# Optimization experiments

Measured on AMD Instinct MI355X. Metric: run time of the kernel, lower is better.

Reference implementation:

```python
import jax, jax.numpy as jnp
import numpy as np

N_NODES = 100000
N_EDGES = 400000
DIM = 3
HID = 32


def _glorot(key, shape):
    fan_in, fan_out = shape[0], shape[1]
    lim = np.sqrt(6.0 / (fan_in + fan_out))
    return jax.random.uniform(key, shape, jnp.float32, -lim, lim)


def setup_inputs() -> dict:
    key = jax.random.key(0)
    ks = jax.random.split(key, 12)
    x = jax.random.normal(ks[0], (N_NODES, DIM), jnp.float32)
    edge_index = jax.random.randint(ks[1], (2, N_EDGES), 0, N_NODES, jnp.int64)
    edge_attr = jax.random.normal(ks[2], (N_EDGES, DIM), jnp.float32)
    params = {
        # conv1: NNConv(3 -> 32), edge nn = Linear(3, 3*32)
        'Wn1': _glorot(ks[3], (DIM, DIM * HID)), 'bn1': jnp.zeros((DIM * HID,), jnp.float32),
        'root1': _glorot(ks[4], (DIM, HID)), 'b1': jnp.zeros((HID,), jnp.float32),
        # conv2: NNConv(32 -> 32), edge nn = Linear(3, 32*32)
        'Wn2': _glorot(ks[5], (DIM, HID * HID)), 'bn2': jnp.zeros((HID * HID,), jnp.float32),
        'root2': _glorot(ks[6], (HID, HID)), 'b2': jnp.zeros((HID,), jnp.float32),
        # fc layers
        'Wf1': _glorot(ks[7], (HID, HID)), 'bf1': jnp.zeros((HID,), jnp.float32),
        'Wf2': _glorot(ks[8], (HID, 1)), 'bf2': jnp.zeros((1,), jnp.float32),
    }
    return {'x': x, 'edge_index': edge_index, 'edge_attr': edge_attr, **params}


def _nnconv(x, src, dst, edge_attr, Wn, bn, root, b, in_c, out_c):
    # per-edge weight matrix from edge MLP: [E, in_c, out_c]
    We = (edge_attr @ Wn + bn).reshape(-1, in_c, out_c)
    # gather source features, per-edge matmul, scatter-add to destinations
    msg = jnp.einsum('ei,eio->eo', x[src], We)  # [E, out_c]
    agg = jax.ops.segment_sum(msg, dst, num_segments=x.shape[0])  # [N, out_c]
    return agg + x @ root + b


def reference(x, edge_index, edge_attr, Wn1, bn1, root1, b1, Wn2, bn2, root2, b2, Wf1, bf1, Wf2, bf2):
    src, dst = edge_index[0], edge_index[1]
    h = jax.nn.relu(_nnconv(x, src, dst, edge_attr, Wn1, bn1, root1, b1, DIM, HID))
    h = jax.nn.relu(_nnconv(h, src, dst, edge_attr, Wn2, bn2, root2, b2, HID, HID))
    h = jax.nn.relu(h @ Wf1 + bf1)
    return h @ Wf2 + bf2  # [N, 1]
```

## Files before the change

### kernel.cpp

```cpp
#include <hip/hip_runtime.h>

#define N_NODES 100000
#define N_EDGES 400000
#define SCAN_BLOCKS ((N_NODES + 255) / 256)

__global__ __launch_bounds__(256) void hist_kernel(const int* __restrict__ ei,
                                                   int* __restrict__ deg) {
    int e = blockIdx.x * 256 + threadIdx.x;
    if (e < N_EDGES) atomicAdd(&deg[ei[N_EDGES + e]], 1);
}

__global__ __launch_bounds__(256) void scanA_kernel(const int* __restrict__ deg,
                                                    int* __restrict__ rowptr,
                                                    int* __restrict__ psum) {
    __shared__ int sm[256];
    int i = blockIdx.x * 256 + threadIdx.x;
    int v = (i < N_NODES) ? deg[i] : 0;
    sm[threadIdx.x] = v;
    __syncthreads();
    #pragma unroll
    for (int off = 1; off < 256; off <<= 1) {
        int t = (threadIdx.x >= off) ? sm[threadIdx.x - off] : 0;
        __syncthreads();
        sm[threadIdx.x] += t;
        __syncthreads();
    }
    if (i < N_NODES) rowptr[i] = sm[threadIdx.x] - v;
    if (threadIdx.x == 255) psum[blockIdx.x] = sm[255];
}

__global__ __launch_bounds__(512) void scanB_kernel(int* __restrict__ psum) {
    __shared__ int sm[512];
    int i = threadIdx.x;
    int v = (i < SCAN_BLOCKS) ? psum[i] : 0;
    sm[i] = v;
    __syncthreads();
    #pragma unroll
    for (int off = 1; off < 512; off <<= 1) {
        int t = (i >= off) ? sm[i - off] : 0;
        __syncthreads();
        sm[i] += t;
        __syncthreads();
    }
    if (i < SCAN_BLOCKS) psum[i] = sm[i];
}

__global__ __launch_bounds__(256) void scanC_kernel(const int* __restrict__ psum,
                                                    int* __restrict__ rowptr,
                                                    int* __restrict__ cursor) {
    int i = blockIdx.x * 256 + threadIdx.x;
    if (i < N_NODES) {
        int base = (blockIdx.x > 0) ? psum[blockIdx.x - 1] : 0;
        int r = rowptr[i] + base;
        rowptr[i] = r;
        cursor[i] = r;
    }
    if (i == 0) rowptr[N_NODES] = N_EDGES;
}

__global__ __launch_bounds__(256) void scatter_kernel(const int* __restrict__ ei,
                                                      const float* __restrict__ ea,
                                                      int* __restrict__ cursor,
                                                      float4* __restrict__ edata) {
    int e = blockIdx.x * 256 + threadIdx.x;
    if (e >= N_EDGES) return;
    int s = ei[e], d = ei[N_EDGES + e];
    int pos = atomicAdd(&cursor[d], 1);
    edata[pos] = make_float4(ea[e*3], ea[e*3+1], ea[e*3+2], __int_as_float(s));
}

__global__ __launch_bounds__(256) void conv1_kernel(const int* __restrict__ rowptr,
                                                    const float4* __restrict__ edata,
                                                    const float* __restrict__ x,
                                                    const float* __restrict__ Wn1,
                                                    const float* __restrict__ bn1,
                                                    const float* __restrict__ root1,
                                                    const float* __restrict__ b1,
                                                    float* __restrict__ h1) {
    int gid = blockIdx.x * 256 + threadIdx.x;
    int n = gid >> 5, o = gid & 31;
    if (n >= N_NODES) return;
    float W[3][3], bb[3];
    #pragma unroll
    for (int d2 = 0; d2 < 3; ++d2)
        #pragma unroll
        for (int d = 0; d < 3; ++d) W[d2][d] = Wn1[d2*96 + d*32 + o];
    #pragma unroll
    for (int d = 0; d < 3; ++d) bb[d] = bn1[d*32 + o];

    float acc = 0.f;
    int j0 = rowptr[n], j1 = rowptr[n + 1];
    for (int j = j0; j < j1; ++j) {
        float4 ed = edata[j];
        int s = __float_as_int(ed.w);
        float x0 = x[s*3], x1 = x[s*3+1], x2 = x[s*3+2];
        float wd0 = fmaf(ed.x, W[0][0], fmaf(ed.y, W[1][0], fmaf(ed.z, W[2][0], bb[0])));
        float wd1 = fmaf(ed.x, W[0][1], fmaf(ed.y, W[1][1], fmaf(ed.z, W[2][1], bb[1])));
        float wd2 = fmaf(ed.x, W[0][2], fmaf(ed.y, W[1][2], fmaf(ed.z, W[2][2], bb[2])));
        acc += fmaf(x0, wd0, fmaf(x1, wd1, x2 * wd2));
    }
    float v = acc + b1[o];
    v = fmaf(x[n*3],   root1[o],      v);
    v = fmaf(x[n*3+1], root1[32 + o], v);
    v = fmaf(x[n*3+2], root1[64 + o], v);
    h1[(size_t)n*32 + o] = fmaxf(v, 0.f);
}

__global__ __launch_bounds__(256) void prep2_kernel(const float* __restrict__ h1,
                                                    const float* __restrict__ Wn2,
                                                    const float* __restrict__ bn2,
                                                    float4* __restrict__ G2) {
    int o = threadIdx.x & 31;
    float w0[32], w1[32], w2[32], w3[32];
    #pragma unroll
    for (int i = 0; i < 32; ++i) {
        w0[i] = Wn2[         i*32 + o];
        w1[i] = Wn2[1024 +   i*32 + o];
        w2[i] = Wn2[2048 +   i*32 + o];
        w3[i] = bn2[         i*32 + o];
    }
    int g = (blockIdx.x * 256 + threadIdx.x) >> 5;
    int gstep = (gridDim.x * 256) >> 5;
    for (int n = g; n < N_NODES; n += gstep) {
        const float* __restrict__ hr = h1 + (size_t)n * 32;
        float g0 = 0.f, g1 = 0.f, g2 = 0.f, g3 = 0.f;
        #pragma unroll
        for (int i = 0; i < 32; ++i) {
            float hi = hr[i];
            g0 = fmaf(hi, w0[i], g0);
            g1 = fmaf(hi, w1[i], g1);
            g2 = fmaf(hi, w2[i], g2);
            g3 = fmaf(hi, w3[i], g3);
        }
        G2[(size_t)n*32 + o] = make_float4(g0, g1, g2, g3);
    }
}

__global__ __launch_bounds__(256) void conv2_kernel(const int* __restrict__ rowptr,
                                                    const float4* __restrict__ edata,
                                                    const float4* __restrict__ G2,
                                                    const float* __restrict__ h1,
                                                    const float* __restrict__ root2,
                                                    const float* __restrict__ b2,
                                                    const float* __restrict__ Wf1,
                                                    const float* __restrict__ bf1,
                                                    const float* __restrict__ Wf2,
                                                    const float* __restrict__ bf2,
                                                    float* __restrict__ out) {
    int gid = blockIdx.x * 256 + threadIdx.x;
    int n = gid >> 5, o = gid & 31;
    if (n >= N_NODES) return;
    float acc = 0.f;
    int j0 = rowptr[n], j1 = rowptr[n + 1];
    for (int j = j0; j < j1; ++j) {
        float4 ed = edata[j];
        int s = __float_as_int(ed.w);
        float4 gg = G2[(size_t)s*32 + o];
        acc += fmaf(ed.x, gg.x, fmaf(ed.y, gg.y, fmaf(ed.z, gg.z, gg.w)));
    }
    const float* __restrict__ hr = h1 + (size_t)n * 32;
    float v = acc + b2[o];
    #pragma unroll
    for (int i = 0; i < 32; ++i) v = fmaf(hr[i], root2[i*32 + o], v);
    float h2 = fmaxf(v, 0.f);

    float a3 = bf1[o];
    #pragma unroll
    for (int i = 0; i < 32; ++i) a3 = fmaf(__shfl(h2, i, 32), Wf1[i*32 + o], a3);
    float h3 = fmaxf(a3, 0.f);

    float p = h3 * Wf2[o];
    #pragma unroll
    for (int off = 16; off; off >>= 1) p += __shfl_down(p, off, 32);
    if (o == 0) out[n] = p + bf2[0];
}

extern "C" void kernel_launch(void* const* d_in, const int* in_sizes, int n_in,
                              void* d_out, int out_size, void* d_ws, size_t ws_size,
                              hipStream_t stream) {
    const float* x     = (const float*)d_in[0];
    const int*   ei    = (const int*)  d_in[1];
    const float* ea    = (const float*)d_in[2];
    const float* Wn1   = (const float*)d_in[3];
    const float* bn1   = (const float*)d_in[4];
    const float* root1 = (const float*)d_in[5];
    const float* b1    = (const float*)d_in[6];
    const float* Wn2   = (const float*)d_in[7];
    const float* bn2   = (const float*)d_in[8];
    const float* root2 = (const float*)d_in[9];
    const float* b2    = (const float*)d_in[10];
    const float* Wf1   = (const float*)d_in[11];
    const float* bf1   = (const float*)d_in[12];
    const float* Wf2   = (const float*)d_in[13];
    const float* bf2   = (const float*)d_in[14];
    float* out = (float*)d_out;

    float*  h1    = (float*)d_ws;
    float4* G2    = (float4*)(h1 + (size_t)N_NODES*32);
    float4* edata = G2 + (size_t)N_NODES*32;
    int*    deg   = (int*)(edata + N_EDGES);
    int*    rowptr= deg + N_NODES;
    int*    cursor= rowptr + N_NODES + 1;
    int*    psum  = cursor + N_NODES;

    hipMemsetAsync(deg, 0, N_NODES * sizeof(int), stream);

    int eb = (N_EDGES + 255) / 256;
    int nb32 = (N_NODES * 32 + 255) / 256;

    hist_kernel   <<<eb, 256, 0, stream>>>(ei, deg);
    scanA_kernel  <<<SCAN_BLOCKS, 256, 0, stream>>>(deg, rowptr, psum);
    scanB_kernel  <<<1, 512, 0, stream>>>(psum);
    scanC_kernel  <<<SCAN_BLOCKS, 256, 0, stream>>>(psum, rowptr, cursor);
    scatter_kernel<<<eb, 256, 0, stream>>>(ei, ea, cursor, edata);
    conv1_kernel  <<<nb32, 256, 0, stream>>>(rowptr, edata, x, Wn1, bn1, root1, b1, h1);
    prep2_kernel  <<<1536, 256, 0, stream>>>(h1, Wn2, bn2, G2);
    conv2_kernel  <<<nb32, 256, 0, stream>>>(rowptr, edata, G2, h1, root2, b2,
                                             Wf1, bf1, Wf2, bf2, out);
}
```

Measured before the change: 169.3 us.

## Merge scan phases, pre-gather source features, unroll edge loops for MLP

Folds the single-block psum scan into the offset-add kernel: each block sums the preceding block totals itself, which removes one launch. The scatter kernel now also writes the gathered source-node x features into a second per-edge array, so conv1 reads them sequentially instead of doing random gathers. The conv1 and conv2 edge loops are unrolled by 2 and 4 with independent accumulators to keep more loads in flight. The costs are an extra per-edge buffer write and redundant psum reads across scan blocks.

```diff
diff --git a/kernel.cpp b/kernel.cpp
--- a/kernel.cpp
+++ b/kernel.cpp
@@ -29,28 +29,20 @@
     if (threadIdx.x == 255) psum[blockIdx.x] = sm[255];
 }
 
-__global__ __launch_bounds__(512) void scanB_kernel(int* __restrict__ psum) {
-    __shared__ int sm[512];
-    int i = threadIdx.x;
-    int v = (i < SCAN_BLOCKS) ? psum[i] : 0;
-    sm[i] = v;
+__global__ __launch_bounds__(256) void scanBC_kernel(const int* __restrict__ psum,
+                                                     int* __restrict__ rowptr,
+                                                     int* __restrict__ cursor) {
+    __shared__ int sm[8];
+    int bid = blockIdx.x, tid = threadIdx.x;
+    int acc = 0;
+    for (int t = tid; t < bid; t += 256) acc += psum[t];
+    #pragma unroll
+    for (int off = 32; off; off >>= 1) acc += __shfl_down(acc, off, 64);
+    if ((tid & 63) == 0) sm[tid >> 6] = acc;
     __syncthreads();
-    #pragma unroll
-    for (int off = 1; off < 512; off <<= 1) {
-        int t = (i >= off) ? sm[i - off] : 0;
-        __syncthreads();
-        sm[i] += t;
-        __syncthreads();
-    }
-    if (i < SCAN_BLOCKS) psum[i] = sm[i];
-}
-
-__global__ __launch_bounds__(256) void scanC_kernel(const int* __restrict__ psum,
-                                                    int* __restrict__ rowptr,
-                                                    int* __restrict__ cursor) {
-    int i = blockIdx.x * 256 + threadIdx.x;
+    int base = sm[0] + sm[1] + sm[2] + sm[3];
+    int i = bid * 256 + tid;
     if (i < N_NODES) {
-        int base = (blockIdx.x > 0) ? psum[blockIdx.x - 1] : 0;
         int r = rowptr[i] + base;
         rowptr[i] = r;
         cursor[i] = r;
@@ -60,17 +52,21 @@
 
 __global__ __launch_bounds__(256) void scatter_kernel(const int* __restrict__ ei,
                                                       const float* __restrict__ ea,
+                                                      const float* __restrict__ x,
                                                       int* __restrict__ cursor,
-                                                      float4* __restrict__ edata) {
+                                                      float4* __restrict__ edataA,
+                                                      float4* __restrict__ edataB) {
     int e = blockIdx.x * 256 + threadIdx.x;
     if (e >= N_EDGES) return;
     int s = ei[e], d = ei[N_EDGES + e];
     int pos = atomicAdd(&cursor[d], 1);
-    edata[pos] = make_float4(ea[e*3], ea[e*3+1], ea[e*3+2], __int_as_float(s));
+    edataA[pos] = make_float4(ea[e*3], ea[e*3+1], ea[e*3+2], __int_as_float(s));
+    edataB[pos] = make_float4(x[s*3], x[s*3+1], x[s*3+2], 0.f);
 }
 
 __global__ __launch_bounds__(256) void conv1_kernel(const int* __restrict__ rowptr,
-                                                    const float4* __restrict__ edata,
+                                                    const float4* __restrict__ edataA,
+                                                    const float4* __restrict__ edataB,
                                                     const float* __restrict__ x,
                                                     const float* __restrict__ Wn1,
                                                     const float* __restrict__ bn1,
@@ -88,18 +84,29 @@
     #pragma unroll
     for (int d = 0; d < 3; ++d) bb[d] = bn1[d*32 + o];
 
-    float acc = 0.f;
     int j0 = rowptr[n], j1 = rowptr[n + 1];
-    for (int j = j0; j < j1; ++j) {
-        float4 ed = edata[j];
-        int s = __float_as_int(ed.w);
-        float x0 = x[s*3], x1 = x[s*3+1], x2 = x[s*3+2];
-        float wd0 = fmaf(ed.x, W[0][0], fmaf(ed.y, W[1][0], fmaf(ed.z, W[2][0], bb[0])));
-        float wd1 = fmaf(ed.x, W[0][1], fmaf(ed.y, W[1][1], fmaf(ed.z, W[2][1], bb[1])));
-        float wd2 = fmaf(ed.x, W[0][2], fmaf(ed.y, W[1][2], fmaf(ed.z, W[2][2], bb[2])));
-        acc += fmaf(x0, wd0, fmaf(x1, wd1, x2 * wd2));
-    }
-    float v = acc + b1[o];
+    float acc0 = 0.f, acc1 = 0.f;
+    int j = j0;
+    for (; j + 2 <= j1; j += 2) {
+        float4 eA0 = edataA[j],   eB0 = edataB[j];
+        float4 eA1 = edataA[j+1], eB1 = edataB[j+1];
+        float wd0 = fmaf(eA0.x, W[0][0], fmaf(eA0.y, W[1][0], fmaf(eA0.z, W[2][0], bb[0])));
+        float wd1 = fmaf(eA0.x, W[0][1], fmaf(eA0.y, W[1][1], fmaf(eA0.z, W[2][1], bb[1])));
+        float wd2 = fmaf(eA0.x, W[0][2], fmaf(eA0.y, W[1][2], fmaf(eA0.z, W[2][2], bb[2])));
+        acc0 += fmaf(eB0.x, wd0, fmaf(eB0.y, wd1, eB0.z * wd2));
+        float ud0 = fmaf(eA1.x, W[0][0], fmaf(eA1.y, W[1][0], fmaf(eA1.z, W[2][0], bb[0])));
+        float ud1 = fmaf(eA1.x, W[0][1], fmaf(eA1.y, W[1][1], fmaf(eA1.z, W[2][1], bb[1])));
+        float ud2 = fmaf(eA1.x, W[0][2], fmaf(eA1.y, W[1][2], fmaf(eA1.z, W[2][2], bb[2])));
+        acc1 += fmaf(eB1.x, ud0, fmaf(eB1.y, ud1, eB1.z * ud2));
+    }
+    if (j < j1) {
+        float4 eA0 = edataA[j], eB0 = edataB[j];
+        float wd0 = fmaf(eA0.x, W[0][0], fmaf(eA0.y, W[1][0], fmaf(eA0.z, W[2][0], bb[0])));
+        float wd1 = fmaf(eA0.x, W[0][1], fmaf(eA0.y, W[1][1], fmaf(eA0.z, W[2][1], bb[1])));
+        float wd2 = fmaf(eA0.x, W[0][2], fmaf(eA0.y, W[1][2], fmaf(eA0.z, W[2][2], bb[2])));
+        acc0 += fmaf(eB0.x, wd0, fmaf(eB0.y, wd1, eB0.z * wd2));
+    }
+    float v = acc0 + acc1 + b1[o];
     v = fmaf(x[n*3],   root1[o],      v);
     v = fmaf(x[n*3+1], root1[32 + o], v);
     v = fmaf(x[n*3+2], root1[64 + o], v);
@@ -137,7 +144,7 @@
 }
 
 __global__ __launch_bounds__(256) void conv2_kernel(const int* __restrict__ rowptr,
-                                                    const float4* __restrict__ edata,
+                                                    const float4* __restrict__ edataA,
                                                     const float4* __restrict__ G2,
                                                     const float* __restrict__ h1,
                                                     const float* __restrict__ root2,
@@ -150,14 +157,28 @@
     int gid = blockIdx.x * 256 + threadIdx.x;
     int n = gid >> 5, o = gid & 31;
     if (n >= N_NODES) return;
-    float acc = 0.f;
     int j0 = rowptr[n], j1 = rowptr[n + 1];
-    for (int j = j0; j < j1; ++j) {
-        float4 ed = edata[j];
-        int s = __float_as_int(ed.w);
-        float4 gg = G2[(size_t)s*32 + o];
-        acc += fmaf(ed.x, gg.x, fmaf(ed.y, gg.y, fmaf(ed.z, gg.z, gg.w)));
-    }
+    float a0 = 0.f, a1 = 0.f, a2 = 0.f, a3v = 0.f;
+    int j = j0;
+    for (; j + 4 <= j1; j += 4) {
+        float4 e0 = edataA[j],   e1 = edataA[j+1];
+        float4 e2 = edataA[j+2], e3 = edataA[j+3];
+        float4 g0 = G2[(size_t)__float_as_int(e0.w)*32 + o];
+        float4 g1 = G2[(size_t)__float_as_int(e1.w)*32 + o];
+        float4 g2 = G2[(size_t)__float_as_int(e2.w)*32 + o];
+        float4 g3 = G2[(size_t)__float_as_int(e3.w)*32 + o];
+        a0 += fmaf(e0.x, g0.x, fmaf(e0.y, g0.y, fmaf(e0.z, g0.z, g0.w)));
+        a1 += fmaf(e1.x, g1.x, fmaf(e1.y, g1.y, fmaf(e1.z, g1.z, g1.w)));
+        a2 += fmaf(e2.x, g2.x, fmaf(e2.y, g2.y, fmaf(e2.z, g2.z, g2.w)));
+        a3v += fmaf(e3.x, g3.x, fmaf(e3.y, g3.y, fmaf(e3.z, g3.z, g3.w)));
+    }
+    for (; j < j1; ++j) {
+        float4 e0 = edataA[j];
+        float4 g0 = G2[(size_t)__float_as_int(e0.w)*32 + o];
+        a0 += fmaf(e0.x, g0.x, fmaf(e0.y, g0.y, fmaf(e0.z, g0.z, g0.w)));
+    }
+    float acc = (a0 + a1) + (a2 + a3v);
+
     const float* __restrict__ hr = h1 + (size_t)n * 32;
     float v = acc + b2[o];
     #pragma unroll
@@ -195,13 +216,14 @@
     const float* bf2   = (const float*)d_in[14];
     float* out = (float*)d_out;
 
-    float*  h1    = (float*)d_ws;
-    float4* G2    = (float4*)(h1 + (size_t)N_NODES*32);
-    float4* edata = G2 + (size_t)N_NODES*32;
-    int*    deg   = (int*)(edata + N_EDGES);
-    int*    rowptr= deg + N_NODES;
-    int*    cursor= rowptr + N_NODES + 1;
-    int*    psum  = cursor + N_NODES;
+    float*  h1     = (float*)d_ws;
+    float4* G2     = (float4*)(h1 + (size_t)N_NODES*32);
+    float4* edataA = G2 + (size_t)N_NODES*32;
+    float4* edataB = edataA + N_EDGES;
+    int*    deg    = (int*)(edataB + N_EDGES);
+    int*    rowptr = deg + N_NODES;
+    int*    cursor = rowptr + N_NODES + 1;
+    int*    psum   = cursor + N_NODES;
 
     hipMemsetAsync(deg, 0, N_NODES * sizeof(int), stream);
 
@@ -210,11 +232,10 @@
 
     hist_kernel   <<<eb, 256, 0, stream>>>(ei, deg);
     scanA_kernel  <<<SCAN_BLOCKS, 256, 0, stream>>>(deg, rowptr, psum);
-    scanB_kernel  <<<1, 512, 0, stream>>>(psum);
-    scanC_kernel  <<<SCAN_BLOCKS, 256, 0, stream>>>(psum, rowptr, cursor);
-    scatter_kernel<<<eb, 256, 0, stream>>>(ei, ea, cursor, edata);
-    conv1_kernel  <<<nb32, 256, 0, stream>>>(rowptr, edata, x, Wn1, bn1, root1, b1, h1);
+    scanBC_kernel <<<SCAN_BLOCKS, 256, 0, stream>>>(psum, rowptr, cursor);
+    scatter_kernel<<<eb, 256, 0, stream>>>(ei, ea, x, cursor, edataA, edataB);
+    conv1_kernel  <<<nb32, 256, 0, stream>>>(rowptr, edataA, edataB, x, Wn1, bn1, root1, b1, h1);
     prep2_kernel  <<<1536, 256, 0, stream>>>(h1, Wn2, bn2, G2);
-    conv2_kernel  <<<nb32, 256, 0, stream>>>(rowptr, edata, G2, h1, root2, b2,
+    conv2_kernel  <<<nb32, 256, 0, stream>>>(rowptr, edataA, G2, h1, root2, b2,
                                              Wf1, bf1, Wf2, bf2, out);
 }
```

Measured after the change: 163.9 us. 1.03x faster.
